# Performance work log

Hardware: AMD Instinct MI355X
Metric: run time of the kernel (lower is better)

## Reference

```python
import jax, jax.numpy as jnp
import numpy as np

B, S, HID = 2, 2048, 2048
NH, NKV, HD = 16, 4, 128
EPS = 1e-6
THETA = 10000.0
NEG = jnp.float32(-1e30)


def setup_inputs() -> dict:
    key = jax.random.key(0)
    ks = jax.random.split(key, 7)
    return {
        "hidden_states": jax.random.normal(ks[0], (B, S, HID), jnp.float32) * 0.02,
        "positions": jnp.broadcast_to(jnp.arange(S, dtype=jnp.int32), (B, S)),
        "Wq": jax.random.normal(ks[1], (HID, NH * HD), jnp.float32) * (HID ** -0.5),
        "Wk": jax.random.normal(ks[2], (HID, NKV * HD), jnp.float32) * (HID ** -0.5),
        "Wv": jax.random.normal(ks[3], (HID, NKV * HD), jnp.float32) * (HID ** -0.5),
        "Wc": jax.random.normal(ks[4], (NH * HD, HID), jnp.float32) * ((NH * HD) ** -0.5),
        "q_scale": jax.random.uniform(ks[5], (HD,), jnp.float32),
        "k_scale": jax.random.uniform(ks[6], (HD,), jnp.float32),
    }


def _rmsnorm(x, scale):
    # per-head RMSNorm over head_dim (nnx.RMSNorm semantics)
    return x * jax.lax.rsqrt(jnp.mean(x * x, axis=-1, keepdims=True) + EPS) * scale


def _rope_neox(x, positions):
    # x: [B, S, H, HD]; full rotary_dim == HD, neox style (split halves)
    half = HD // 2
    inv_freq = 1.0 / (THETA ** (jnp.arange(half, dtype=jnp.float32) / half))
    ang = positions[..., None].astype(jnp.float32) * inv_freq  # [B, S, half]
    cos = jnp.cos(ang)[:, :, None, :]
    sin = jnp.sin(ang)[:, :, None, :]
    x1, x2 = jnp.split(x, 2, axis=-1)
    return jnp.concatenate([x1 * cos - x2 * sin, x2 * cos + x1 * sin], axis=-1)


def reference(hidden_states, positions, Wq, Wk, Wv, Wc, q_scale, k_scale):
    q = (hidden_states @ Wq).reshape(B, S, NH, HD)
    k = (hidden_states @ Wk).reshape(B, S, NKV, HD)
    v = (hidden_states @ Wv).reshape(B, S, NKV, HD)
    q = _rmsnorm(q, q_scale)
    k = _rmsnorm(k, k_scale)
    q = _rope_neox(q, positions)
    k = _rope_neox(k, positions)
    # GQA: expand KV heads to query heads
    rep = NH // NKV
    k = jnp.repeat(k, rep, axis=2)
    v = jnp.repeat(v, rep, axis=2)
    scores = jnp.einsum("bqhd,bkhd->bhqk", q, k) * (HD ** -0.5)
    causal = jnp.tril(jnp.ones((S, S), dtype=bool))
    scores = jnp.where(causal, scores, NEG)
    probs = jax.nn.softmax(scores, axis=-1)
    attn = jnp.einsum("bhqk,bkhd->bqhd", probs, v).reshape(B, S, NH * HD)
    return attn @ Wc
```

## Files before the change

### kernel.cpp

```cpp
#include <hip/hip_runtime.h>
#include <stdint.h>

typedef unsigned short u16;
typedef unsigned int u32;
typedef __bf16 bf16x8 __attribute__((ext_vector_type(8)));
typedef float f32x4 __attribute__((ext_vector_type(4)));
typedef u32 u32x4 __attribute__((ext_vector_type(4)));

__device__ __forceinline__ u16 f2bf(float x){
  u32 u = __float_as_uint(x);
  u += 0x7FFFu + ((u >> 16) & 1u);
  return (u16)(u >> 16);
}
__device__ __forceinline__ float bf2f(u16 h){
  return __uint_as_float(((u32)h) << 16);
}
__device__ __forceinline__ u32 cvt_pk_bf16(float lo, float hi){
  u32 r;
  asm("v_cvt_pk_bf16_f32 %0, %1, %2" : "=v"(r) : "v"(lo), "v"(hi));
  return r;
}
__device__ __forceinline__ f32x4 mfma16(bf16x8 a, bf16x8 b, f32x4 c){
  return __builtin_amdgcn_mfma_f32_16x16x32_bf16(a, b, c, 0, 0, 0);
}
__device__ __forceinline__ void gload16(const void* g, const void* l){
  __builtin_amdgcn_global_load_lds(
      (__attribute__((address_space(1))) void*)(uintptr_t)g,
      (__attribute__((address_space(3))) void*)(u32)(uintptr_t)l,
      16, 0, 0);
}

__global__ __launch_bounds__(256) void k_prep(const float* __restrict__ hidden,
    const float* __restrict__ Wq, const float* __restrict__ Wk, const float* __restrict__ Wv,
    const float* __restrict__ Wc, u16* __restrict__ hid_bf, u16* __restrict__ wqkv_t,
    u16* __restrict__ wct, float* __restrict__ ct, float* __restrict__ st){
  __shared__ float tile[32][33];
  int bid = blockIdx.x;
  int t = threadIdx.x;
  if (bid < 8192){
    int i = (bid * 256 + t) * 4;
    float4 v = *(const float4*)(hidden + i);
    ushort4 o;
    o.x = f2bf(v.x); o.y = f2bf(v.y); o.z = f2bf(v.z); o.w = f2bf(v.w);
    *(ushort4*)(hid_bf + i) = o;
    return;
  }
  if (bid < 8192 + 6144){
    int b2 = bid - 8192;
    int nb = (b2 % 96) * 32, kb = (b2 / 96) * 32;
    int tx = t & 31, ty = t >> 5;
    #pragma unroll
    for (int j = 0; j < 4; j++){
      int k = kb + ty + j*8;
      int n = nb + tx;
      float v;
      if (n < 2048)      v = Wq[(size_t)k*2048 + n];
      else if (n < 2560) v = Wk[(size_t)k*512 + (n - 2048)];
      else               v = Wv[(size_t)k*512 + (n - 2560)];
      tile[tx][ty + j*8] = v;
    }
    __syncthreads();
    #pragma unroll
    for (int j = 0; j < 4; j++){
      int n = nb + ty + j*8;
      wqkv_t[(size_t)n*2048 + kb + tx] = f2bf(tile[ty + j*8][tx]);
    }
    return;
  }
  if (bid < 8192 + 6144 + 4096){
    int b3 = bid - 8192 - 6144;
    int nb = (b3 % 64) * 32, kb = (b3 / 64) * 32;
    int tx = t & 31, ty = t >> 5;
    #pragma unroll
    for (int j = 0; j < 4; j++){
      tile[tx][ty + j*8] = Wc[(size_t)(kb + ty + j*8)*2048 + nb + tx];
    }
    __syncthreads();
    #pragma unroll
    for (int j = 0; j < 4; j++){
      wct[(size_t)(nb + ty + j*8)*2048 + kb + tx] = f2bf(tile[ty + j*8][tx]);
    }
    return;
  }
  {
    int b4 = bid - 8192 - 6144 - 4096;
    int idx = b4 * 256 + t;
    int p = idx >> 6, i = idx & 63;
    float freq = powf(10000.0f, -(float)i / 64.0f);
    float ang = (float)p * freq;
    ct[idx] = cosf(ang);
    st[idx] = sinf(ang);
  }
}

__global__ __launch_bounds__(256) void k_gemm_qkv(const u16* __restrict__ A, const u16* __restrict__ Bt,
    u16* __restrict__ qkv, u16* __restrict__ vt, int K){
  __shared__ u16 lds[16384];
  int tid = threadIdx.x;
  int lane = tid & 63, w = tid >> 6;
  int g = lane >> 4, c16 = lane & 15;
  int wr = w >> 1, wc = w & 1;
  int chunk = gridDim.x >> 3;
  int logical = (blockIdx.x & 7) * chunk + (blockIdx.x >> 3);
  int bx = logical % 24, by = logical / 24;
  size_t bm = (size_t)by * 128, bn = (size_t)bx * 128;
  f32x4 zero = {0.f, 0.f, 0.f, 0.f};
  f32x4 acc[4][4];
  #pragma unroll
  for (int i=0;i<4;i++)
    #pragma unroll
    for (int j=0;j<4;j++) acc[i][j] = zero;

  int jj = (w*2)*64 + lane;
  const int nt = K >> 5;
  #pragma unroll
  for (int p = 0; p < 2; p++){
    int j = jj + p*64;
    int r = j >> 2, slot = j & 3;
    gload16(A  + (bm + r)*(size_t)K + slot*8, (const char*)(lds)        + (w*2+p)*1024);
    gload16(Bt + (bn + r)*(size_t)K + slot*8, (const char*)(lds + 8192) + (w*2+p)*1024);
  }
  asm volatile("s_waitcnt vmcnt(0)" ::: "memory");
  __builtin_amdgcn_s_barrier();

  int cur = 0;
  #pragma unroll 1
  for (int t = 0; t < nt; ++t){
    if (t + 1 < nt){
      int k0 = (t + 1) << 5;
      #pragma unroll
      for (int p = 0; p < 2; p++){
        int j = jj + p*64;
        int r = j >> 2, slot = j & 3;
        gload16(A  + (bm + r)*(size_t)K + k0 + slot*8, (const char*)(lds + (cur^1)*4096)        + (w*2+p)*1024);
        gload16(Bt + (bn + r)*(size_t)K + k0 + slot*8, (const char*)(lds + 8192 + (cur^1)*4096) + (w*2+p)*1024);
      }
    }
    const u16* Ac = lds + cur*4096;
    const u16* Bc = lds + 8192 + cur*4096;
    bf16x8 af[4], bfr[4];
    #pragma unroll
    for (int mi=0;mi<4;mi++) af[mi]  = *(const bf16x8*)&Ac[(wr*64 + mi*16 + c16)*32 + g*8];
    #pragma unroll
    for (int ni=0;ni<4;ni++) bfr[ni] = *(const bf16x8*)&Bc[(wc*64 + ni*16 + c16)*32 + g*8];
    #pragma unroll
    for (int mi=0;mi<4;mi++)
      #pragma unroll
      for (int ni=0;ni<4;ni++)
        acc[mi][ni] = mfma16(af[mi], bfr[ni], acc[mi][ni]);
    if (t + 1 < nt){
      asm volatile("s_waitcnt vmcnt(0)" ::: "memory");
      __builtin_amdgcn_s_barrier();
    }
    cur ^= 1;
  }
  if (bx < 20){
    #pragma unroll
    for (int mi=0;mi<4;mi++){
      #pragma unroll
      for (int ni=0;ni<4;ni++){
        #pragma unroll
        for (int r=0;r<4;r++){
          size_t row = bm + wr*64 + mi*16 + g*4 + r;
          size_t col = bn + wc*64 + ni*16 + c16;
          qkv[row * (size_t)3072 + col] = f2bf(acc[mi][ni][r]);
        }
      }
    }
  } else {
    __syncthreads();
    #pragma unroll
    for (int mi=0;mi<4;mi++)
      #pragma unroll
      for (int ni=0;ni<4;ni++)
        #pragma unroll
        for (int r=0;r<4;r++){
          int row = wr*64 + mi*16 + g*4 + r;
          int col = wc*64 + ni*16 + c16;
          lds[col*128 + row] = f2bf(acc[mi][ni][r]);
        }
    __syncthreads();
    int b = (int)(bm >> 11), s0 = (int)(bm & 2047);
    int kvh = bx - 20;
    u16* dst0 = vt + ((size_t)(b*4 + kvh) * 128) * 2048 + s0;
    #pragma unroll
    for (int i = 0; i < 8; i++){
      int ch = i*256 + tid;
      int d = ch >> 4;
      int off = (ch & 15) * 8;
      uint4 vv = *(uint4*)&lds[d*128 + off];
      *(uint4*)(dst0 + (size_t)d*2048 + off) = vv;
    }
  }
}

template<bool OBF>
__global__ __launch_bounds__(256) void k_gemm(const u16* __restrict__ A, const u16* __restrict__ Bt,
                                              void* __restrict__ Cv, int M, int N, int K, int nbx){
  __shared__ u16 As[2][128*32], Bs[2][128*32];
  int tid = threadIdx.x;
  int lane = tid & 63, w = tid >> 6;
  int g = lane >> 4, c16 = lane & 15;
  int wr = w >> 1, wc = w & 1;
  int chunk = gridDim.x >> 3;
  int logical = (blockIdx.x & 7) * chunk + (blockIdx.x >> 3);
  int bx = logical % nbx, by = logical / nbx;
  size_t bm = (size_t)by * 128, bn = (size_t)bx * 128;
  f32x4 zero = {0.f, 0.f, 0.f, 0.f};
  f32x4 acc[4][4];
  #pragma unroll
  for (int i=0;i<4;i++)
    #pragma unroll
    for (int j=0;j<4;j++) acc[i][j] = zero;

  int jj = (w*2)*64 + lane;
  int nt = K >> 5;
  #pragma unroll
  for (int p = 0; p < 2; p++){
    int j = jj + p*64;
    int r = j >> 2, slot = j & 3;
    gload16(A  + (bm + r)*(size_t)K + slot*8, (const char*)As[0] + (w*2+p)*1024);
    gload16(Bt + (bn + r)*(size_t)K + slot*8, (const char*)Bs[0] + (w*2+p)*1024);
  }
  asm volatile("s_waitcnt vmcnt(0)" ::: "memory");
  __builtin_amdgcn_s_barrier();

  int cur = 0;
  #pragma unroll 1
  for (int t = 0; t < nt; ++t){
    if (t + 1 < nt){
      int k0 = (t + 1) << 5;
      #pragma unroll
      for (int p = 0; p < 2; p++){
        int j = jj + p*64;
        int r = j >> 2, slot = j & 3;
        gload16(A  + (bm + r)*(size_t)K + k0 + slot*8, (const char*)As[cur^1] + (w*2+p)*1024);
        gload16(Bt + (bn + r)*(size_t)K + k0 + slot*8, (const char*)Bs[cur^1] + (w*2+p)*1024);
      }
    }
    const u16* Ac = As[cur];
    const u16* Bc = Bs[cur];
    bf16x8 af[4], bfr[4];
    #pragma unroll
    for (int mi=0;mi<4;mi++) af[mi]  = *(const bf16x8*)&Ac[(wr*64 + mi*16 + c16)*32 + g*8];
    #pragma unroll
    for (int ni=0;ni<4;ni++) bfr[ni] = *(const bf16x8*)&Bc[(wc*64 + ni*16 + c16)*32 + g*8];
    #pragma unroll
    for (int mi=0;mi<4;mi++)
      #pragma unroll
      for (int ni=0;ni<4;ni++)
        acc[mi][ni] = mfma16(af[mi], bfr[ni], acc[mi][ni]);
    if (t + 1 < nt){
      asm volatile("s_waitcnt vmcnt(0)" ::: "memory");
      __builtin_amdgcn_s_barrier();
    }
    cur ^= 1;
  }
  #pragma unroll
  for (int mi=0;mi<4;mi++){
    #pragma unroll
    for (int ni=0;ni<4;ni++){
      #pragma unroll
      for (int r=0;r<4;r++){
        size_t row = bm + wr*64 + mi*16 + g*4 + r;
        size_t col = bn + wc*64 + ni*16 + c16;
        if (OBF) ((u16*)Cv)[row * (size_t)N + col] = f2bf(acc[mi][ni][r]);
        else     ((float*)Cv)[row * (size_t)N + col] = acc[mi][ni][r];
      }
    }
  }
}

__global__ __launch_bounds__(256) void k_norm_rope(const u16* __restrict__ qkv, const int* __restrict__ pos,
    const float* __restrict__ qsc, const float* __restrict__ ksc,
    const float* __restrict__ ct, const float* __restrict__ st,
    u16* __restrict__ qo, u16* __restrict__ ko){
  int bs = blockIdx.x;
  int hh = blockIdx.y * 4 + (threadIdx.x >> 6);
  int d = threadIdx.x & 63;
  int b = bs >> 11, s = bs & 2047;
  const u16* row = qkv + (size_t)bs * 3072 + hh * 128;
  u16 r1 = row[d], r2 = row[d + 64];
  float x1 = bf2f(r1), x2 = bf2f(r2);
  float ssq = x1*x1 + x2*x2;
  #pragma unroll
  for (int mm = 1; mm < 64; mm <<= 1) ssq += __shfl_xor(ssq, mm);
  float inv = rsqrtf(ssq * (1.0f/128.0f) + 1e-6f);
  const float* sc = (hh < 16) ? qsc : ksc;
  float y1 = x1 * inv * sc[d];
  float y2 = x2 * inv * sc[d + 64];
  int p = pos[bs];
  float c = ct[p*64 + d], sn = st[p*64 + d];
  float o1 = y1*c - y2*sn;
  float o2 = y2*c + y1*sn;
  if (hh < 16){
    o1 *= 0.1275174528f;
    o2 *= 0.1275174528f;
    size_t o = ((size_t)(b*16 + hh) * 2048 + s) * 128 + d;
    qo[o] = f2bf(o1); qo[o + 64] = f2bf(o2);
  } else {
    size_t o = ((size_t)(b*4 + (hh-16)) * 2048 + s) * 128 + d;
    ko[o] = f2bf(o1); ko[o + 64] = f2bf(o2);
  }
}

__device__ __forceinline__ void stage_kv8(int w, int lane, u16* ksb, u16* vsb,
                                          const u16* kp, const u16* vp, int c0){
  #pragma unroll
  for (int p = 0; p < 2; p++){
    int j = (w*2 + p)*64 + lane;
    int r = j >> 4, slot = j & 15;
    gload16(kp + (size_t)(c0 + r)*128 + ((slot ^ (r & 7)) << 3),
            (const char*)ksb + (w*2 + p)*1024);
  }
  #pragma unroll
  for (int p = 0; p < 2; p++){
    int j = (w*2 + p)*64 + lane;
    int r = j >> 3, slot = j & 7;
    gload16(vp + (size_t)r*2048 + c0 + ((slot ^ (r & 7)) << 3),
            (const char*)vsb + (w*2 + p)*1024);
  }
}

__device__ __forceinline__ void sm_frags(f32x4 (&sacc)[4],
    int qrow, bool diag, int c0, int g, int c16, u32x4* pw){
  if (diag){
    #pragma unroll
    for (int nt = 0; nt < 4; nt++)
      #pragma unroll
      for (int r = 0; r < 4; r++)
        if (c0 + nt*16 + g*4 + r > qrow) sacc[nt][r] = -1e30f;
  }
  #pragma unroll
  for (int nt = 0; nt < 4; nt++)
    #pragma unroll
    for (int r = 0; r < 4; r++)
      sacc[nt][r] = exp2f(sacc[nt][r]);
  u32 pkA[4], pkB[4];
  #pragma unroll
  for (int a = 0; a < 4; a++){
    pkA[a] = cvt_pk_bf16(sacc[a][0], sacc[a][1]);
    pkB[a] = cvt_pk_bf16(sacc[a][2], sacc[a][3]);
  }
  int s0l = (((g*2    ) & 3) << 4) | c16;
  int s1l = (((g*2 + 1) & 3) << 4) | c16;
  bool hi = (g & 2) != 0;
  u32 v0A[4], v0B[4], v1A[4], v1B[4];
  #pragma unroll
  for (int a = 0; a < 4; a++){
    v0A[a] = (u32)__shfl((int)pkA[a], s0l);
    v0B[a] = (u32)__shfl((int)pkB[a], s0l);
    v1A[a] = (u32)__shfl((int)pkA[a], s1l);
    v1B[a] = (u32)__shfl((int)pkB[a], s1l);
  }
  #pragma unroll
  for (int kk2 = 0; kk2 < 2; kk2++){
    pw[kk2].x = hi ? v0A[2*kk2+1] : v0A[2*kk2];
    pw[kk2].y = hi ? v0B[2*kk2+1] : v0B[2*kk2];
    pw[kk2].z = hi ? v1A[2*kk2+1] : v1A[2*kk2];
    pw[kk2].w = hi ? v1B[2*kk2+1] : v1B[2*kk2];
  }
}

__global__ __launch_bounds__(512, 2) void k_attn(const u16* __restrict__ q, const u16* __restrict__ k,
    const u16* __restrict__ vt, u16* __restrict__ attn){
  __shared__ u16 Ks[2][64*128];
  __shared__ u16 Vs[2][128*64];
  int lane = threadIdx.x & 63, w = threadIdx.x >> 6;
  int g = lane >> 4, c16 = lane & 15;
  int bid = blockIdx.x;
  int logical = (bid & 7)*32 + (bid >> 3);
  int pi = logical & 7;
  int hb = logical >> 3;
  int h = hb & 15, b = hb >> 4;
  int kvh = h >> 2;
  int qbA = pi*128, qbB = (15 - pi)*128;
  int tA = 2*pi + 1;
  int tmax = 31 - 2*pi;
  const u16* qp = q  + ((size_t)(b*16 + h))  * 2048 * 128;
  const u16* kp = k  + ((size_t)(b*4 + kvh)) * 2048 * 128;
  const u16* vp = vt + ((size_t)(b*4 + kvh)) * 128 * 2048;

  int qrA = qbA + w*16 + c16, qrB = qbB + w*16 + c16;
  bf16x8 qfA[4], qfB[4];
  #pragma unroll
  for (int kk = 0; kk < 4; kk++){
    qfA[kk] = *(const bf16x8*)(qp + (size_t)qrA*128 + kk*32 + g*8);
    qfB[kk] = *(const bf16x8*)(qp + (size_t)qrB*128 + kk*32 + g*8);
  }
  asm volatile("s_waitcnt vmcnt(0)" ::: "memory");

  u32x4 onesw = {0x3F803F80u, 0x3F803F80u, 0x3F803F80u, 0x3F803F80u};
  bf16x8 ones = __builtin_bit_cast(bf16x8, onesw);

  f32x4 zero = {0.f,0.f,0.f,0.f};
  f32x4 oA[8], oB[8];
  #pragma unroll
  for (int i=0;i<8;i++){ oA[i] = zero; oB[i] = zero; }
  f32x4 lA = zero, lB = zero;

  stage_kv8(w, lane, Ks[0], Vs[0], kp, vp, 0);

  for (int t = 0; t <= tmax; t++){
    int c0 = t*64;
    if (t < tmax){
      stage_kv8(w, lane, Ks[(t+1)&1], Vs[(t+1)&1], kp, vp, c0 + 64);
      asm volatile("s_waitcnt vmcnt(4)" ::: "memory");
    } else {
      asm volatile("s_waitcnt vmcnt(0)" ::: "memory");
    }
    __builtin_amdgcn_s_barrier();
    const u16* ksb = Ks[t&1];
    const u16* vsb = Vs[t&1];
    bool Aact = (t <= tA);
    f32x4 sA[4], sB[4];
    #pragma unroll
    for (int i=0;i<4;i++){ sA[i] = zero; sB[i] = zero; }
    __builtin_amdgcn_s_setprio(1);
    if (Aact){
      #pragma unroll
      for (int nt=0;nt<4;nt++){
        #pragma unroll
        for (int kk=0;kk<4;kk++){
          int row = nt*16 + c16;
          bf16x8 kf = *(const bf16x8*)&ksb[row*128 + (((kk*4 + g) ^ (row & 7)) << 3)];
          sB[nt] = mfma16(kf, qfB[kk], sB[nt]);
          sA[nt] = mfma16(kf, qfA[kk], sA[nt]);
        }
      }
    } else {
      #pragma unroll
      for (int nt=0;nt<4;nt++){
        #pragma unroll
        for (int kk=0;kk<4;kk++){
          int row = nt*16 + c16;
          bf16x8 kf = *(const bf16x8*)&ksb[row*128 + (((kk*4 + g) ^ (row & 7)) << 3)];
          sB[nt] = mfma16(kf, qfB[kk], sB[nt]);
        }
      }
    }
    __builtin_amdgcn_s_setprio(0);
    u32x4 pwA[2], pwB[2];
    if (Aact) sm_frags(sA, qrA, t >= 2*pi,     c0, g, c16, pwA);
    sm_frags(sB, qrB, t >= tmax - 1, c0, g, c16, pwB);
    __builtin_amdgcn_s_setprio(1);
    if (Aact){
      #pragma unroll
      for (int kk2 = 0; kk2 < 2; kk2++){
        bf16x8 pfA = __builtin_bit_cast(bf16x8, pwA[kk2]);
        bf16x8 pfB = __builtin_bit_cast(bf16x8, pwB[kk2]);
        lA = mfma16(pfA, ones, lA);
        lB = mfma16(pfB, ones, lB);
        #pragma unroll
        for (int dt = 0; dt < 8; dt++){
          int d = dt*16 + c16;
          bf16x8 vf = *(const bf16x8*)&vsb[d*64 + (((kk2*4 + g) ^ (d & 7)) << 3)];
          oB[dt] = mfma16(pfB, vf, oB[dt]);
          oA[dt] = mfma16(pfA, vf, oA[dt]);
        }
      }
    } else {
      #pragma unroll
      for (int kk2 = 0; kk2 < 2; kk2++){
        bf16x8 pfB = __builtin_bit_cast(bf16x8, pwB[kk2]);
        lB = mfma16(pfB, ones, lB);
        #pragma unroll
        for (int dt = 0; dt < 8; dt++){
          int d = dt*16 + c16;
          bf16x8 vf = *(const bf16x8*)&vsb[d*64 + (((kk2*4 + g) ^ (d & 7)) << 3)];
          oB[dt] = mfma16(pfB, vf, oB[dt]);
        }
      }
    }
    __builtin_amdgcn_s_setprio(0);
    __builtin_amdgcn_sched_barrier(0);
    asm volatile("s_waitcnt lgkmcnt(0)" ::: "memory");
    __builtin_amdgcn_s_barrier();
  }
  float invA[4], invB[4];
  #pragma unroll
  for (int r = 0; r < 4; r++){
    invA[r] = 1.0f / lA[r];
    invB[r] = 1.0f / lB[r];
  }
  #pragma unroll
  for (int dt=0;dt<8;dt++){
    #pragma unroll
    for (int r=0;r<4;r++){
      size_t orA = (size_t)b*2048 + qbA + w*16 + g*4 + r;
      size_t orB = (size_t)b*2048 + qbB + w*16 + g*4 + r;
      attn[orA*2048 + (size_t)h*128 + dt*16 + c16] = f2bf(oA[dt][r] * invA[r]);
      attn[orB*2048 + (size_t)h*128 + dt*16 + c16] = f2bf(oB[dt][r] * invB[r]);
    }
  }
}

extern "C" void kernel_launch(void* const* d_in, const int* in_sizes, int n_in,
                              void* d_out, int out_size, void* d_ws, size_t ws_size,
                              hipStream_t stream){
  const float* hidden    = (const float*)d_in[0];
  const int*   positions = (const int*)d_in[1];
  const float* Wq = (const float*)d_in[2];
  const float* Wk = (const float*)d_in[3];
  const float* Wv = (const float*)d_in[4];
  const float* Wc = (const float*)d_in[5];
  const float* qs = (const float*)d_in[6];
  const float* ks = (const float*)d_in[7];
  float* out = (float*)d_out;
  char* ws = (char*)d_ws;
  float* ct      = (float*)(ws + 0);
  float* st      = (float*)(ws + 524288);
  u16*   hid_bf  = (u16*)(ws + 1048576);
  u16*   attn_bf = hid_bf;
  u16*   wqkv_t  = (u16*)(ws + 17825792);
  u16*   wct     = (u16*)(ws + 30408704);
  u16*   qkv_bf  = (u16*)(ws + 38797312);
  u16*   q_bf    = (u16*)(ws + 63963136);
  u16*   k_bf    = (u16*)(ws + 80740352);
  u16*   vt_bf   = (u16*)(ws + 84934656);

  k_prep<<<18944, 256, 0, stream>>>(hidden, Wq, Wk, Wv, Wc, hid_bf, wqkv_t, wct, ct, st);
  k_gemm_qkv<<<768, 256, 0, stream>>>(hid_bf, wqkv_t, qkv_bf, vt_bf, 2048);
  k_norm_rope<<<dim3(4096, 5), 256, 0, stream>>>(qkv_bf, positions, qs, ks, ct, st, q_bf, k_bf);
  k_attn<<<256, 512, 0, stream>>>(q_bf, k_bf, vt_bf, attn_bf);
  k_gemm<false><<<512, 256, 0, stream>>>(attn_bf, wct, (void*)out, 4096, 2048, 2048, 16);
}
```

Measured before the change: 206.6 us.

## Fuse QK RMSNorm and RoPE into the QKV GEMM epilogue

The per-head RMSNorm, scaling and NeoX RoPE now run inside the QKV GEMM epilogue, since each 128-column tile is exactly one head. Row sums of squares are reduced across lanes and waves through LDS, and the normalized tile is staged in LDS so each element can read its rotary partner. This removes the separate norm/rope kernel launch and the round trip of the bf16 qkv intermediate through global memory. In exchange the epilogue gains extra barriers and scattered cos/sin table reads, and the normalized values are rounded to bf16 before rotation.

```diff
diff --git a/kernel.cpp b/kernel.cpp
--- a/kernel.cpp
+++ b/kernel.cpp
@@ -94,7 +94,9 @@
 }
 
 __global__ __launch_bounds__(256) void k_gemm_qkv(const u16* __restrict__ A, const u16* __restrict__ Bt,
-    u16* __restrict__ qkv, u16* __restrict__ vt, int K){
+    const int* __restrict__ pos, const float* __restrict__ qsc, const float* __restrict__ ksc,
+    const float* __restrict__ ct, const float* __restrict__ st,
+    u16* __restrict__ qo, u16* __restrict__ ko, u16* __restrict__ vt, int K){
   __shared__ u16 lds[16384];
   int tid = threadIdx.x;
   int lane = tid & 63, w = tid >> 6;
@@ -154,21 +156,73 @@
     }
     cur ^= 1;
   }
-  if (bx < 20){
+  __syncthreads();
+  int hh = bx;
+  int b = (int)(bm >> 11);
+  int s0 = (int)(bm & 2047);
+  if (hh < 20){
+    float* ssq = (float*)lds;
     #pragma unroll
     for (int mi=0;mi<4;mi++){
       #pragma unroll
-      for (int ni=0;ni<4;ni++){
+      for (int r=0;r<4;r++){
+        float s2 = 0.f;
+        #pragma unroll
+        for (int ni=0;ni<4;ni++){ float v = acc[mi][ni][r]; s2 += v*v; }
+        s2 += __shfl_xor(s2, 1);
+        s2 += __shfl_xor(s2, 2);
+        s2 += __shfl_xor(s2, 4);
+        s2 += __shfl_xor(s2, 8);
+        if (c16 == 0) ssq[(wr*64 + mi*16 + g*4 + r)*2 + wc] = s2;
+      }
+    }
+    __syncthreads();
+    float inv[4][4];
+    #pragma unroll
+    for (int mi=0;mi<4;mi++)
+      #pragma unroll
+      for (int r=0;r<4;r++){
+        int row = wr*64 + mi*16 + g*4 + r;
+        inv[mi][r] = rsqrtf((ssq[row*2] + ssq[row*2+1]) * (1.0f/128.0f) + 1e-6f);
+      }
+    __syncthreads();
+    const float* scp = (hh < 16) ? qsc : ksc;
+    float qmul = (hh < 16) ? 0.1275174528f : 1.0f;
+    float scv[4];
+    #pragma unroll
+    for (int ni=0;ni<4;ni++) scv[ni] = scp[wc*64 + ni*16 + c16] * qmul;
+    #pragma unroll
+    for (int mi=0;mi<4;mi++)
+      #pragma unroll
+      for (int ni=0;ni<4;ni++)
         #pragma unroll
         for (int r=0;r<4;r++){
-          size_t row = bm + wr*64 + mi*16 + g*4 + r;
-          size_t col = bn + wc*64 + ni*16 + c16;
-          qkv[row * (size_t)3072 + col] = f2bf(acc[mi][ni][r]);
+          int row = wr*64 + mi*16 + g*4 + r;
+          int col = wc*64 + ni*16 + c16;
+          lds[row*128 + col] = f2bf(acc[mi][ni][r] * inv[mi][r] * scv[ni]);
+        }
+    __syncthreads();
+    u16* outp = (hh < 16) ? (qo + ((size_t)(b*16 + hh) * 2048 + s0) * 128)
+                          : (ko + ((size_t)(b*4 + (hh-16)) * 2048 + s0) * 128);
+    #pragma unroll
+    for (int mi=0;mi<4;mi++){
+      #pragma unroll
+      for (int r=0;r<4;r++){
+        int row = wr*64 + mi*16 + g*4 + r;
+        int p = pos[bm + row];
+        #pragma unroll
+        for (int ni=0;ni<4;ni++){
+          int col = wc*64 + ni*16 + c16;
+          int i = col & 63;
+          float cc = ct[p*64 + i], sn = st[p*64 + i];
+          float own = bf2f(lds[row*128 + col]);
+          float oth = bf2f(lds[row*128 + (col ^ 64)]);
+          float outv = (col < 64) ? (own*cc - oth*sn) : (own*cc + oth*sn);
+          outp[(size_t)row*128 + col] = f2bf(outv);
         }
       }
     }
   } else {
-    __syncthreads();
     #pragma unroll
     for (int mi=0;mi<4;mi++)
       #pragma unroll
@@ -180,8 +234,7 @@
           lds[col*128 + row] = f2bf(acc[mi][ni][r]);
         }
     __syncthreads();
-    int b = (int)(bm >> 11), s0 = (int)(bm & 2047);
-    int kvh = bx - 20;
+    int kvh = hh - 20;
     u16* dst0 = vt + ((size_t)(b*4 + kvh) * 128) * 2048 + s0;
     #pragma unroll
     for (int i = 0; i < 8; i++){
@@ -268,39 +321,6 @@
         else     ((float*)Cv)[row * (size_t)N + col] = acc[mi][ni][r];
       }
     }
-  }
-}
-
-__global__ __launch_bounds__(256) void k_norm_rope(const u16* __restrict__ qkv, const int* __restrict__ pos,
-    const float* __restrict__ qsc, const float* __restrict__ ksc,
-    const float* __restrict__ ct, const float* __restrict__ st,
-    u16* __restrict__ qo, u16* __restrict__ ko){
-  int bs = blockIdx.x;
-  int hh = blockIdx.y * 4 + (threadIdx.x >> 6);
-  int d = threadIdx.x & 63;
-  int b = bs >> 11, s = bs & 2047;
-  const u16* row = qkv + (size_t)bs * 3072 + hh * 128;
-  u16 r1 = row[d], r2 = row[d + 64];
-  float x1 = bf2f(r1), x2 = bf2f(r2);
-  float ssq = x1*x1 + x2*x2;
-  #pragma unroll
-  for (int mm = 1; mm < 64; mm <<= 1) ssq += __shfl_xor(ssq, mm);
-  float inv = rsqrtf(ssq * (1.0f/128.0f) + 1e-6f);
-  const float* sc = (hh < 16) ? qsc : ksc;
-  float y1 = x1 * inv * sc[d];
-  float y2 = x2 * inv * sc[d + 64];
-  int p = pos[bs];
-  float c = ct[p*64 + d], sn = st[p*64 + d];
-  float o1 = y1*c - y2*sn;
-  float o2 = y2*c + y1*sn;
-  if (hh < 16){
-    o1 *= 0.1275174528f;
-    o2 *= 0.1275174528f;
-    size_t o = ((size_t)(b*16 + hh) * 2048 + s) * 128 + d;
-    qo[o] = f2bf(o1); qo[o + 64] = f2bf(o2);
-  } else {
-    size_t o = ((size_t)(b*4 + (hh-16)) * 2048 + s) * 128 + d;
-    ko[o] = f2bf(o1); ko[o + 64] = f2bf(o2);
   }
 }
 
@@ -514,14 +534,12 @@
   u16*   attn_bf = hid_bf;
   u16*   wqkv_t  = (u16*)(ws + 17825792);
   u16*   wct     = (u16*)(ws + 30408704);
-  u16*   qkv_bf  = (u16*)(ws + 38797312);
   u16*   q_bf    = (u16*)(ws + 63963136);
   u16*   k_bf    = (u16*)(ws + 80740352);
   u16*   vt_bf   = (u16*)(ws + 84934656);
 
   k_prep<<<18944, 256, 0, stream>>>(hidden, Wq, Wk, Wv, Wc, hid_bf, wqkv_t, wct, ct, st);
-  k_gemm_qkv<<<768, 256, 0, stream>>>(hid_bf, wqkv_t, qkv_bf, vt_bf, 2048);
-  k_norm_rope<<<dim3(4096, 5), 256, 0, stream>>>(qkv_bf, positions, qs, ks, ct, st, q_bf, k_bf);
+  k_gemm_qkv<<<768, 256, 0, stream>>>(hid_bf, wqkv_t, positions, qs, ks, ct, st, q_bf, k_bf, vt_bf, 2048);
   k_attn<<<256, 512, 0, stream>>>(q_bf, k_bf, vt_bf, attn_bf);
   k_gemm<false><<<512, 256, 0, stream>>>(attn_bf, wct, (void*)out, 4096, 2048, 2048, 16);
 }
```

After: 216.2 us. 1.05x slower.

## Split attention work so each wave group owns one 64-row causal query tile

Applied to the files above, without the earlier changes.

The attention kernel now launches 512 blocks instead of 256. Each block pairs a low and a high 64-row query tile, and the two halves of the 8 waves each handle one tile. Before, every wave processed two 16-row query strips from paired 128-row tiles. The change raises block count and parallelism across CUs and halves per-wave accumulator registers, which may improve occupancy. The cost is that K/V tiles are staged into shared memory by twice as many blocks, and the waves working the short tile sit idle after their causal cutoff while the other group finishes.

```diff
diff --git a/kernel.cpp b/kernel.cpp
--- a/kernel.cpp
+++ b/kernel.cpp
@@ -368,36 +368,36 @@
   __shared__ u16 Vs[2][128*64];
   int lane = threadIdx.x & 63, w = threadIdx.x >> 6;
   int g = lane >> 4, c16 = lane & 15;
+  int wg = w >> 2;
+  int wi = w & 3;
   int bid = blockIdx.x;
-  int logical = (bid & 7)*32 + (bid >> 3);
-  int pi = logical & 7;
-  int hb = logical >> 3;
+  int logical = (bid & 7)*64 + (bid >> 3);
+  int pi = logical & 15;
+  int hb = logical >> 4;
   int h = hb & 15, b = hb >> 4;
   int kvh = h >> 2;
-  int qbA = pi*128, qbB = (15 - pi)*128;
-  int tA = 2*pi + 1;
-  int tmax = 31 - 2*pi;
+  int qb   = wg ? (31 - pi)*64 : pi*64;
+  int tact = wg ? (31 - pi)     : pi;
+  int tmax = 31 - pi;
   const u16* qp = q  + ((size_t)(b*16 + h))  * 2048 * 128;
   const u16* kp = k  + ((size_t)(b*4 + kvh)) * 2048 * 128;
   const u16* vp = vt + ((size_t)(b*4 + kvh)) * 128 * 2048;
 
-  int qrA = qbA + w*16 + c16, qrB = qbB + w*16 + c16;
-  bf16x8 qfA[4], qfB[4];
-  #pragma unroll
-  for (int kk = 0; kk < 4; kk++){
-    qfA[kk] = *(const bf16x8*)(qp + (size_t)qrA*128 + kk*32 + g*8);
-    qfB[kk] = *(const bf16x8*)(qp + (size_t)qrB*128 + kk*32 + g*8);
-  }
+  int qrow = qb + wi*16 + c16;
+  bf16x8 qf[4];
+  #pragma unroll
+  for (int kk = 0; kk < 4; kk++)
+    qf[kk] = *(const bf16x8*)(qp + (size_t)qrow*128 + kk*32 + g*8);
   asm volatile("s_waitcnt vmcnt(0)" ::: "memory");
 
   u32x4 onesw = {0x3F803F80u, 0x3F803F80u, 0x3F803F80u, 0x3F803F80u};
   bf16x8 ones = __builtin_bit_cast(bf16x8, onesw);
 
   f32x4 zero = {0.f,0.f,0.f,0.f};
-  f32x4 oA[8], oB[8];
-  #pragma unroll
-  for (int i=0;i<8;i++){ oA[i] = zero; oB[i] = zero; }
-  f32x4 lA = zero, lB = zero;
+  f32x4 o[8];
+  #pragma unroll
+  for (int i=0;i<8;i++) o[i] = zero;
+  f32x4 l = zero;
 
   stage_kv8(w, lane, Ks[0], Vs[0], kp, vp, 0);
 
@@ -412,85 +412,50 @@
     __builtin_amdgcn_s_barrier();
     const u16* ksb = Ks[t&1];
     const u16* vsb = Vs[t&1];
-    bool Aact = (t <= tA);
-    f32x4 sA[4], sB[4];
-    #pragma unroll
-    for (int i=0;i<4;i++){ sA[i] = zero; sB[i] = zero; }
-    __builtin_amdgcn_s_setprio(1);
-    if (Aact){
+    if (t <= tact){
+      f32x4 sacc[4];
+      #pragma unroll
+      for (int i=0;i<4;i++) sacc[i] = zero;
+      __builtin_amdgcn_s_setprio(1);
       #pragma unroll
       for (int nt=0;nt<4;nt++){
         #pragma unroll
         for (int kk=0;kk<4;kk++){
           int row = nt*16 + c16;
           bf16x8 kf = *(const bf16x8*)&ksb[row*128 + (((kk*4 + g) ^ (row & 7)) << 3)];
-          sB[nt] = mfma16(kf, qfB[kk], sB[nt]);
-          sA[nt] = mfma16(kf, qfA[kk], sA[nt]);
+          sacc[nt] = mfma16(kf, qf[kk], sacc[nt]);
         }
       }
-    } else {
-      #pragma unroll
-      for (int nt=0;nt<4;nt++){
-        #pragma unroll
-        for (int kk=0;kk<4;kk++){
-          int row = nt*16 + c16;
-          bf16x8 kf = *(const bf16x8*)&ksb[row*128 + (((kk*4 + g) ^ (row & 7)) << 3)];
-          sB[nt] = mfma16(kf, qfB[kk], sB[nt]);
-        }
-      }
-    }
-    __builtin_amdgcn_s_setprio(0);
-    u32x4 pwA[2], pwB[2];
-    if (Aact) sm_frags(sA, qrA, t >= 2*pi,     c0, g, c16, pwA);
-    sm_frags(sB, qrB, t >= tmax - 1, c0, g, c16, pwB);
-    __builtin_amdgcn_s_setprio(1);
-    if (Aact){
+      __builtin_amdgcn_s_setprio(0);
+      u32x4 pw[2];
+      sm_frags(sacc, qrow, t == tact, c0, g, c16, pw);
+      __builtin_amdgcn_s_setprio(1);
       #pragma unroll
       for (int kk2 = 0; kk2 < 2; kk2++){
-        bf16x8 pfA = __builtin_bit_cast(bf16x8, pwA[kk2]);
-        bf16x8 pfB = __builtin_bit_cast(bf16x8, pwB[kk2]);
-        lA = mfma16(pfA, ones, lA);
-        lB = mfma16(pfB, ones, lB);
+        bf16x8 pf = __builtin_bit_cast(bf16x8, pw[kk2]);
+        l = mfma16(pf, ones, l);
         #pragma unroll
         for (int dt = 0; dt < 8; dt++){
           int d = dt*16 + c16;
           bf16x8 vf = *(const bf16x8*)&vsb[d*64 + (((kk2*4 + g) ^ (d & 7)) << 3)];
-          oB[dt] = mfma16(pfB, vf, oB[dt]);
-          oA[dt] = mfma16(pfA, vf, oA[dt]);
+          o[dt] = mfma16(pf, vf, o[dt]);
         }
       }
-    } else {
-      #pragma unroll
-      for (int kk2 = 0; kk2 < 2; kk2++){
-        bf16x8 pfB = __builtin_bit_cast(bf16x8, pwB[kk2]);
-        lB = mfma16(pfB, ones, lB);
-        #pragma unroll
-        for (int dt = 0; dt < 8; dt++){
-          int d = dt*16 + c16;
-          bf16x8 vf = *(const bf16x8*)&vsb[d*64 + (((kk2*4 + g) ^ (d & 7)) << 3)];
-          oB[dt] = mfma16(pfB, vf, oB[dt]);
-        }
-      }
-    }
-    __builtin_amdgcn_s_setprio(0);
+      __builtin_amdgcn_s_setprio(0);
+    }
     __builtin_amdgcn_sched_barrier(0);
     asm volatile("s_waitcnt lgkmcnt(0)" ::: "memory");
     __builtin_amdgcn_s_barrier();
   }
-  float invA[4], invB[4];
-  #pragma unroll
-  for (int r = 0; r < 4; r++){
-    invA[r] = 1.0f / lA[r];
-    invB[r] = 1.0f / lB[r];
-  }
+  float inv[4];
+  #pragma unroll
+  for (int r = 0; r < 4; r++) inv[r] = 1.0f / l[r];
   #pragma unroll
   for (int dt=0;dt<8;dt++){
     #pragma unroll
     for (int r=0;r<4;r++){
-      size_t orA = (size_t)b*2048 + qbA + w*16 + g*4 + r;
-      size_t orB = (size_t)b*2048 + qbB + w*16 + g*4 + r;
-      attn[orA*2048 + (size_t)h*128 + dt*16 + c16] = f2bf(oA[dt][r] * invA[r]);
-      attn[orB*2048 + (size_t)h*128 + dt*16 + c16] = f2bf(oB[dt][r] * invB[r]);
+      size_t orow = (size_t)b*2048 + qb + wi*16 + g*4 + r;
+      attn[orow*2048 + (size_t)h*128 + dt*16 + c16] = f2bf(o[dt][r] * inv[r]);
     }
   }
 }
@@ -522,6 +487,6 @@
   k_prep<<<18944, 256, 0, stream>>>(hidden, Wq, Wk, Wv, Wc, hid_bf, wqkv_t, wct, ct, st);
   k_gemm_qkv<<<768, 256, 0, stream>>>(hid_bf, wqkv_t, qkv_bf, vt_bf, 2048);
   k_norm_rope<<<dim3(4096, 5), 256, 0, stream>>>(qkv_bf, positions, qs, ks, ct, st, q_bf, k_bf);
-  k_attn<<<256, 512, 0, stream>>>(q_bf, k_bf, vt_bf, attn_bf);
+  k_attn<<<512, 512, 0, stream>>>(q_bf, k_bf, vt_bf, attn_bf);
   k_gemm<false><<<512, 256, 0, stream>>>(attn_bf, wct, (void*)out, 4096, 2048, 2048, 16);
 }
```

Measured after the change: 206.9 us. Within noise of the previous version (+0.1%).

## Permute K row mapping in QK^T so P fragments need no cross-lane shuffles

Applied to the files above, without the earlier changes.

Changes which K rows each MFMA tile covers so that the score accumulator layout already matches the A-operand layout needed for the PV MFMA. This removes the per-iteration ds_bpermute shuffles and selects in the softmax packing step. The LDS swizzle for K is adjusted to match the new row mapping, and the causal mask column indices are remapped. The risk is LDS bank conflicts under the new swizzle, or an indexing mistake that breaks correctness.

```diff
diff --git a/kernel.cpp b/kernel.cpp
--- a/kernel.cpp
+++ b/kernel.cpp
@@ -310,7 +310,8 @@
   for (int p = 0; p < 2; p++){
     int j = (w*2 + p)*64 + lane;
     int r = j >> 4, slot = j & 15;
-    gload16(kp + (size_t)(c0 + r)*128 + ((slot ^ (r & 7)) << 3),
+    int swzr = (r & 3) | ((r >> 1) & 4);
+    gload16(kp + (size_t)(c0 + r)*128 + ((slot ^ swzr) << 3),
             (const char*)ksb + (w*2 + p)*1024);
   }
   #pragma unroll
@@ -322,43 +323,27 @@
   }
 }
 
-__device__ __forceinline__ void sm_frags(f32x4 (&sacc)[4],
-    int qrow, bool diag, int c0, int g, int c16, u32x4* pw){
+__device__ __forceinline__ void pack_group(f32x4 (&sacc)[4],
+    int qrow, bool diag, int c0, int g, u32x4* pw){
   if (diag){
     #pragma unroll
     for (int nt = 0; nt < 4; nt++)
       #pragma unroll
       for (int r = 0; r < 4; r++)
-        if (c0 + nt*16 + g*4 + r > qrow) sacc[nt][r] = -1e30f;
+        if (c0 + ((nt >> 1) << 5) + ((nt & 1) << 2) + 8*g + r > qrow)
+          sacc[nt][r] = -1e30f;
   }
   #pragma unroll
   for (int nt = 0; nt < 4; nt++)
     #pragma unroll
     for (int r = 0; r < 4; r++)
       sacc[nt][r] = exp2f(sacc[nt][r]);
-  u32 pkA[4], pkB[4];
-  #pragma unroll
-  for (int a = 0; a < 4; a++){
-    pkA[a] = cvt_pk_bf16(sacc[a][0], sacc[a][1]);
-    pkB[a] = cvt_pk_bf16(sacc[a][2], sacc[a][3]);
-  }
-  int s0l = (((g*2    ) & 3) << 4) | c16;
-  int s1l = (((g*2 + 1) & 3) << 4) | c16;
-  bool hi = (g & 2) != 0;
-  u32 v0A[4], v0B[4], v1A[4], v1B[4];
-  #pragma unroll
-  for (int a = 0; a < 4; a++){
-    v0A[a] = (u32)__shfl((int)pkA[a], s0l);
-    v0B[a] = (u32)__shfl((int)pkB[a], s0l);
-    v1A[a] = (u32)__shfl((int)pkA[a], s1l);
-    v1B[a] = (u32)__shfl((int)pkB[a], s1l);
-  }
   #pragma unroll
   for (int kk2 = 0; kk2 < 2; kk2++){
-    pw[kk2].x = hi ? v0A[2*kk2+1] : v0A[2*kk2];
-    pw[kk2].y = hi ? v0B[2*kk2+1] : v0B[2*kk2];
-    pw[kk2].z = hi ? v1A[2*kk2+1] : v1A[2*kk2];
-    pw[kk2].w = hi ? v1B[2*kk2+1] : v1B[2*kk2];
+    pw[kk2].x = cvt_pk_bf16(sacc[2*kk2][0],   sacc[2*kk2][1]);
+    pw[kk2].y = cvt_pk_bf16(sacc[2*kk2][2],   sacc[2*kk2][3]);
+    pw[kk2].z = cvt_pk_bf16(sacc[2*kk2+1][0], sacc[2*kk2+1][1]);
+    pw[kk2].w = cvt_pk_bf16(sacc[2*kk2+1][2], sacc[2*kk2+1][3]);
   }
 }
 
@@ -393,6 +378,9 @@
   u32x4 onesw = {0x3F803F80u, 0x3F803F80u, 0x3F803F80u, 0x3F803F80u};
   bf16x8 ones = __builtin_bit_cast(bf16x8, onesw);
 
+  int rb = 8*(c16 >> 2) + (c16 & 3);
+  int cs = c16 & 7;
+
   f32x4 zero = {0.f,0.f,0.f,0.f};
   f32x4 oA[8], oB[8];
   #pragma unroll
@@ -420,10 +408,10 @@
     if (Aact){
       #pragma unroll
       for (int nt=0;nt<4;nt++){
+        int R = ((nt >> 1) << 5) + ((nt & 1) << 2) + rb;
         #pragma unroll
         for (int kk=0;kk<4;kk++){
-          int row = nt*16 + c16;
-          bf16x8 kf = *(const bf16x8*)&ksb[row*128 + (((kk*4 + g) ^ (row & 7)) << 3)];
+          bf16x8 kf = *(const bf16x8*)&ksb[R*128 + (((kk*4 + g) ^ cs) << 3)];
           sB[nt] = mfma16(kf, qfB[kk], sB[nt]);
           sA[nt] = mfma16(kf, qfA[kk], sA[nt]);
         }
@@ -431,18 +419,18 @@
     } else {
       #pragma unroll
       for (int nt=0;nt<4;nt++){
+        int R = ((nt >> 1) << 5) + ((nt & 1) << 2) + rb;
         #pragma unroll
         for (int kk=0;kk<4;kk++){
-          int row = nt*16 + c16;
-          bf16x8 kf = *(const bf16x8*)&ksb[row*128 + (((kk*4 + g) ^ (row & 7)) << 3)];
+          bf16x8 kf = *(const bf16x8*)&ksb[R*128 + (((kk*4 + g) ^ cs) << 3)];
           sB[nt] = mfma16(kf, qfB[kk], sB[nt]);
         }
       }
     }
     __builtin_amdgcn_s_setprio(0);
     u32x4 pwA[2], pwB[2];
-    if (Aact) sm_frags(sA, qrA, t >= 2*pi,     c0, g, c16, pwA);
-    sm_frags(sB, qrB, t >= tmax - 1, c0, g, c16, pwB);
+    if (Aact) pack_group(sA, qrA, t >= 2*pi,     c0, g, pwA);
+    pack_group(sB, qrB, t >= tmax - 1, c0, g, pwB);
     __builtin_amdgcn_s_setprio(1);
     if (Aact){
       #pragma unroll
```

New measurement: 199.9 us. 1.03x faster.
